# Kernel optimization log

Hardware: AMD Instinct MI355X
Metric: run time of the kernel (lower is better)

Reference implementation:

```python
import jax, jax.numpy as jnp
import numpy as np

E, N, D, H = 600000, 100000, 128, 128
LN_EPS = 1e-5


def setup_inputs() -> dict:
    key = jax.random.key(0)
    ks = jax.random.split(key, 10)
    inp = {
        "efeat": jax.random.normal(ks[0], (E, D), dtype=jnp.float32),
        "nfeat": jax.random.normal(ks[1], (N, D), dtype=jnp.float32),
        "src_idx": jax.random.randint(ks[2], (E,), 0, N, dtype=jnp.int64) if jax.config.jax_enable_x64 else jax.random.randint(ks[2], (E,), 0, N, dtype=jnp.int32),
        "dst_idx": jax.random.randint(ks[3], (E,), 0, N, dtype=jnp.int32),
        # MLP params: Linear(3D -> H) + SiLU, Linear(H -> D), LayerNorm(D)
        "W1": jax.random.normal(ks[4], (3 * D, H), dtype=jnp.float32) / np.sqrt(3 * D),
        "b1": jnp.zeros((H,), dtype=jnp.float32),
        "W2": jax.random.normal(ks[5], (H, D), dtype=jnp.float32) / np.sqrt(H),
        "b2": jnp.zeros((D,), dtype=jnp.float32),
        "ln_scale": jnp.ones((D,), dtype=jnp.float32),
        "ln_bias": jnp.zeros((D,), dtype=jnp.float32),
    }
    return inp


def _layernorm(x, scale, bias):
    mu = jnp.mean(x, axis=-1, keepdims=True)
    var = jnp.mean(jnp.square(x - mu), axis=-1, keepdims=True)
    return (x - mu) * jax.lax.rsqrt(var + LN_EPS) * scale + bias


def reference(efeat, nfeat, src_idx, dst_idx, W1, b1, W2, b2, ln_scale, ln_bias):
    # Gather per-edge source/destination node features (irregular access).
    src = nfeat[src_idx]              # [E, D]
    dst = nfeat[dst_idx]              # [E, D]
    # TMLP: equivalent to concat([efeat, src, dst]) @ W1; expressed as split GEMMs
    # so no [E, 3D] concat buffer is materialized.
    Wf, Ws, Wd = W1[:D], W1[D:2 * D], W1[2 * D:]
    h = efeat @ Wf + src @ Ws + dst @ Wd + b1   # [E, H]
    h = jax.nn.silu(h)
    y = h @ W2 + b2                              # [E, D]
    y = _layernorm(y, ln_scale, ln_bias)
    efeat_new = y + efeat                        # residual add
    return (efeat_new, nfeat)
```

## Files before the change

### kernel.cpp

```cpp
#include <hip/hip_runtime.h>
#include <stdint.h>

#define E_N 600000
#define N_N 100000

typedef short short8   __attribute__((ext_vector_type(8)));
typedef short short8a  __attribute__((ext_vector_type(8), may_alias));
typedef float floatx2  __attribute__((ext_vector_type(2)));
typedef float floatx4  __attribute__((ext_vector_type(4)));
typedef float floatx16 __attribute__((ext_vector_type(16)));
typedef float floatx4a __attribute__((ext_vector_type(4), may_alias));
typedef float floatx8a __attribute__((ext_vector_type(8), may_alias));
typedef unsigned int uintx2  __attribute__((ext_vector_type(2)));
typedef unsigned int uintx4  __attribute__((ext_vector_type(4)));
typedef unsigned int uintx4a __attribute__((ext_vector_type(4), may_alias));
typedef __bf16 bf16x4 __attribute__((ext_vector_type(4)));
typedef __bf16 bf16x8 __attribute__((ext_vector_type(8)));

static __device__ __forceinline__ unsigned short f2bf(float f){
  unsigned u = __builtin_bit_cast(unsigned, f);
  unsigned rnd = 0x7fffu + ((u >> 16) & 1u);
  return (unsigned short)((u + rnd) >> 16);
}
static __device__ __forceinline__ unsigned pk2(float a, float b){
  floatx2 f; f[0] = a; f[1] = b;
  typedef __bf16 bf16x2 __attribute__((ext_vector_type(2)));
  return __builtin_bit_cast(unsigned, __builtin_convertvector(f, bf16x2));
}

__global__ void prep_weights(const float* __restrict__ W1, const float* __restrict__ W2,
                             unsigned short* __restrict__ wall){
  int i = blockIdx.x * 256 + threadIdx.x;
  int c, k, win; float v;
  if (i < 384 * 128){
    c = i / 384; k = i - c * 384; win = k >> 6;
    v = W1[k * 128 + c];
  } else {
    int j = i - 384 * 128;
    c = j >> 7; k = j & 127; win = 6 + (k >> 6);
    v = W2[k * 128 + c];
  }
  int kp = k & 63;
  wall[win * 8192 + (c * 32 + ((kp >> 1) ^ ((c & 7) << 2))) * 2 + (kp & 1)] = f2bf(v);
}

__global__ void prep_nfeat(const float* __restrict__ nf,
                           unsigned* __restrict__ nfbu,
                           float* __restrict__ out2){
  const int total = N_N * 128 / 4;
  int stride = gridDim.x * blockDim.x;
  for (int i = blockIdx.x * blockDim.x + threadIdx.x; i < total; i += stride){
    float4 v = reinterpret_cast<const float4*>(nf)[i];
    reinterpret_cast<float4*>(out2)[i] = v;
    nfbu[2 * i]     = pk2(v.x, v.y);
    nfbu[2 * i + 1] = pk2(v.z, v.w);
  }
}

static __device__ __forceinline__ void glds16(void* lds, const void* g){
  __builtin_amdgcn_global_load_lds((const __attribute__((address_space(1))) unsigned int*)g,
                                   (__attribute__((address_space(3))) unsigned int*)lds,
                                   16, 0, 0);
}

__global__ __launch_bounds__(256, 3) void fused_edge(
    const float* __restrict__ efeat,
    const int* __restrict__ src_idx, const int* __restrict__ dst_idx,
    const unsigned short* __restrict__ nfb,
    const unsigned short* __restrict__ wall,
    const float* __restrict__ b1, const float* __restrict__ b2,
    const float* __restrict__ lns, const float* __restrict__ lnb,
    float* __restrict__ out)
{
  __shared__ __align__(16) unsigned char smem[34816];
  unsigned int* wbuf  = (unsigned int*)smem;
  float*        cmisc = (float*)(smem + 32768);

  const int tid  = threadIdx.x;
  const int w    = tid >> 6;
  const int lane = tid & 63;
  const int rl   = lane & 31;
  const int hi   = lane >> 5;
  const int swz  = (rl & 7) << 2;

  auto stageW = [&](int b, int win){
    const unsigned char* src = (const unsigned char*)wall + win * 16384;
    #pragma unroll
    for (int rnd = 0; rnd < 4; ++rnd){
      int off = rnd * 4096 + tid * 16;
      glds16(smem + b * 16384 + off, src + off);
    }
  };

  stageW(0, 0);
  cmisc[tid]       = tid < 128 ? b1[tid]  : b2[tid - 128];
  cmisc[tid + 256] = tid < 128 ? lns[tid] : lnb[tid - 128];

  const int e0 = blockIdx.x * 128 + w * 32 + rl;
  const int ec = e0 < E_N ? e0 : (E_N - 1);
  int si = src_idx[ec], di = dst_idx[ec];
  si = si < 0 ? 0 : (si >= N_N ? N_N - 1 : si);
  di = di < 0 ? 0 : (di >= N_N ? N_N - 1 : di);

  auto ldE = [&](int ks8) -> short8 {
    floatx8a f = *reinterpret_cast<const floatx8a*>(efeat + (size_t)ec * 128 + ks8 * 16 + hi * 8);
    return __builtin_bit_cast(short8, __builtin_convertvector(f, bf16x8));
  };
  auto ldG = [&](int row, int ks8) -> short8 {
    return *reinterpret_cast<const short8a*>(nfb + (size_t)row * 128 + ks8 * 16 + hi * 8);
  };

  short8 xe[8], xc[4], xn[4];
  #pragma unroll
  for (int ks8 = 0; ks8 < 8; ++ks8) xe[ks8] = ldE(ks8);
  #pragma unroll
  for (int k = 0; k < 4; ++k) xc[k] = ldG(si, k);

  __syncthreads();

  auto loadW = [&](int b, int m, int ks) -> short8 {
    uintx4a v = *reinterpret_cast<const uintx4a*>(
        &wbuf[b * 4096 + (32 * m + rl) * 32 + ((ks * 8 + hi * 4) ^ swz)]);
    return __builtin_bit_cast(short8, v);
  };

  floatx16 acc1[4];
  #pragma unroll
  for (int mt = 0; mt < 4; ++mt)
    #pragma unroll
    for (int q = 0; q < 16; ++q) acc1[mt][q] = 0.f;

  auto g1win = [&](int b, const short8* xs){
    #pragma unroll
    for (int ks = 0; ks < 4; ++ks){
      #pragma unroll
      for (int mt = 0; mt < 4; ++mt){
        short8 wf = loadW(b, mt, ks);
        acc1[mt] = __builtin_amdgcn_mfma_f32_32x32x16_bf16(wf, xs[ks], acc1[mt], 0, 0, 0);
      }
    }
  };

  stageW(1, 1);
  #pragma unroll
  for (int k = 0; k < 4; ++k) xn[k] = ldG(si, 4 + k);
  g1win(0, xe);
  __syncthreads();

  stageW(0, 2);
  g1win(1, xe + 4);
  __syncthreads();

  stageW(1, 3);
  g1win(0, xc);
  #pragma unroll
  for (int k = 0; k < 4; ++k) xc[k] = ldG(di, k);
  __syncthreads();

  stageW(0, 4);
  g1win(1, xn);
  #pragma unroll
  for (int k = 0; k < 4; ++k) xn[k] = ldG(di, 4 + k);
  __syncthreads();

  stageW(1, 5);
  g1win(0, xc);
  __syncthreads();

  stageW(0, 6);
  g1win(1, xn);
  __syncthreads();

  short8 hfr[8];
  #pragma unroll
  for (int mt = 0; mt < 4; ++mt){
    floatx4 sv[4];
    #pragma unroll
    for (int p = 0; p < 4; ++p){
      floatx4 bb = *reinterpret_cast<const floatx4a*>(&cmisc[32 * mt + 8 * p + 4 * hi]);
      #pragma unroll
      for (int i = 0; i < 4; ++i){
        float xx = acc1[mt][4 * p + i] + bb[i];
        sv[p][i] = xx * __builtin_amdgcn_rcpf(1.f + __expf(-xx));
      }
    }
    #pragma unroll
    for (int k1 = 0; k1 < 2; ++k1){
      uintx2 P0 = __builtin_bit_cast(uintx2, __builtin_convertvector(sv[2 * k1],     bf16x4));
      uintx2 P1 = __builtin_bit_cast(uintx2, __builtin_convertvector(sv[2 * k1 + 1], bf16x4));
      unsigned sA = hi ? P0[0] : P1[0];
      unsigned sB = hi ? P0[1] : P1[1];
      unsigned rA = __shfl_xor(sA, 32);
      unsigned rB = __shfl_xor(sB, 32);
      uintx4 u;
      u[0] = hi ? rA : P0[0];
      u[1] = hi ? rB : P0[1];
      u[2] = hi ? P1[0] : rA;
      u[3] = hi ? P1[1] : rB;
      hfr[2 * mt + k1] = __builtin_bit_cast(short8, u);
    }
  }

  uintx2 rk[8], rr[8];
  #pragma unroll
  for (int ks = 0; ks < 8; ++ks){
    uintx4 u = __builtin_bit_cast(uintx4, xe[ks]);
    unsigned sA = hi ? u[0] : u[2];
    unsigned sB = hi ? u[1] : u[3];
    rr[ks][0] = __shfl_xor(sA, 32);
    rr[ks][1] = __shfl_xor(sB, 32);
    rk[ks][0] = hi ? u[2] : u[0];
    rk[ks][1] = hi ? u[3] : u[1];
  }

  floatx16 acc2[4];
  #pragma unroll
  for (int mo = 0; mo < 4; ++mo)
    #pragma unroll
    for (int q = 0; q < 16; ++q) acc2[mo][q] = 0.f;

  stageW(1, 7);
  #pragma unroll
  for (int ks = 0; ks < 4; ++ks)
    #pragma unroll
    for (int mo = 0; mo < 4; ++mo)
      acc2[mo] = __builtin_amdgcn_mfma_f32_32x32x16_bf16(loadW(0, mo, ks), hfr[ks], acc2[mo], 0, 0, 0);
  __syncthreads();
  #pragma unroll
  for (int ks = 0; ks < 4; ++ks)
    #pragma unroll
    for (int mo = 0; mo < 4; ++mo)
      acc2[mo] = __builtin_amdgcn_mfma_f32_32x32x16_bf16(loadW(1, mo, ks), hfr[4 + ks], acc2[mo], 0, 0, 0);

  float s1 = 0.f, s2 = 0.f;
  #pragma unroll
  for (int mt = 0; mt < 4; ++mt)
    #pragma unroll
    for (int p = 0; p < 4; ++p){
      floatx4 bb = *reinterpret_cast<const floatx4a*>(&cmisc[128 + 32 * mt + 8 * p + 4 * hi]);
      #pragma unroll
      for (int i = 0; i < 4; ++i){
        float v = acc2[mt][4 * p + i] + bb[i];
        s1 += v; s2 += v * v;
      }
    }
  s1 += __shfl_xor(s1, 32); s2 += __shfl_xor(s2, 32);

  float mu   = s1 * (1.f / 128.f);
  float var  = s2 * (1.f / 128.f) - mu * mu;
  var = var > 0.f ? var : 0.f;
  float rstd = __builtin_amdgcn_rsqf(var + 1e-5f);

  if (e0 < E_N){
    float* op = out + (size_t)e0 * 128;
    #pragma unroll
    for (int mt = 0; mt < 4; ++mt)
      #pragma unroll
      for (int p = 0; p < 4; ++p){
        int c = 32 * mt + 8 * p + 4 * hi;
        floatx4 bb = *reinterpret_cast<const floatx4a*>(&cmisc[128 + c]);
        floatx4 ls = *reinterpret_cast<const floatx4a*>(&cmisc[256 + c]);
        floatx4 lb = *reinterpret_cast<const floatx4a*>(&cmisc[384 + c]);
        const int ks = 2 * mt + (p >> 1);
        uintx2 pk_ = ((p & 1) == hi) ? rk[ks] : rr[ks];
        floatx4 o4;
        #pragma unroll
        for (int i = 0; i < 4; ++i){
          unsigned dwv = pk_[i >> 1];
          float ef = __builtin_bit_cast(float, (i & 1) ? (dwv & 0xffff0000u) : (dwv << 16));
          o4[i] = (acc2[mt][4 * p + i] + bb[i] - mu) * rstd * ls[i] + lb[i] + ef;
        }
        *reinterpret_cast<floatx4a*>(op + c) = o4;
      }
  }
}

extern "C" void kernel_launch(void* const* d_in, const int* in_sizes, int n_in,
                              void* d_out, int out_size, void* d_ws, size_t ws_size,
                              hipStream_t stream){
  const float* efeat = (const float*)d_in[0];
  const float* nfeat = (const float*)d_in[1];
  const int*   srci  = (const int*)d_in[2];
  const int*   dsti  = (const int*)d_in[3];
  const float* W1    = (const float*)d_in[4];
  const float* b1    = (const float*)d_in[5];
  const float* W2    = (const float*)d_in[6];
  const float* b2    = (const float*)d_in[7];
  const float* lns   = (const float*)d_in[8];
  const float* lnb   = (const float*)d_in[9];
  float* out = (float*)d_out;

  char* ws = (char*)d_ws;
  unsigned short* wall = (unsigned short*)ws;
  unsigned short* nfb  = (unsigned short*)(ws + 131072);

  prep_weights<<<(384 * 128 + 128 * 128) / 256, 256, 0, stream>>>(W1, W2, wall);
  prep_nfeat<<<2048, 256, 0, stream>>>(nfeat, (unsigned*)nfb, out + (size_t)E_N * 128);

  int blocks = (E_N + 127) / 128;
  fused_edge<<<blocks, 256, 0, stream>>>(efeat, srci, dsti, nfb, wall,
                                         b1, b2, lns, lnb, out);
}
```

Before: 231.1 us.

## Triple-buffer weight windows with manual vmcnt barriers and MFMA priority

Grows LDS from two to three 16KB weight buffers so weight staging runs two windows ahead. Full __syncthreads are replaced by s_waitcnt vmcnt(N) plus s_barrier, so outstanding node-feature gathers are not drained at each barrier. The gathers are restructured into two rotating register sets, and s_setprio raises wave priority around MFMA loops. The larger LDS footprint (50KB per block) may limit occupancy under launch_bounds(256,3), and the hand-counted vmcnt values must match the actual number of loads in flight for correctness.

```diff
diff --git a/kernel.cpp b/kernel.cpp
--- a/kernel.cpp
+++ b/kernel.cpp
@@ -28,6 +28,15 @@
   return __builtin_bit_cast(unsigned, __builtin_convertvector(f, bf16x2));
 }
 
+#define WAITBAR(N) do{ \
+  asm volatile("s_waitcnt vmcnt(" #N ")" ::: "memory"); \
+  __builtin_amdgcn_s_barrier(); \
+  asm volatile("" ::: "memory"); }while(0)
+#define BARONLY() do{ \
+  asm volatile("" ::: "memory"); \
+  __builtin_amdgcn_s_barrier(); \
+  asm volatile("" ::: "memory"); }while(0)
+
 __global__ void prep_weights(const float* __restrict__ W1, const float* __restrict__ W2,
                              unsigned short* __restrict__ wall){
   int i = blockIdx.x * 256 + threadIdx.x;
@@ -72,9 +81,9 @@
     const float* __restrict__ lns, const float* __restrict__ lnb,
     float* __restrict__ out)
 {
-  __shared__ __align__(16) unsigned char smem[34816];
+  __shared__ __align__(16) unsigned char smem[51200];
   unsigned int* wbuf  = (unsigned int*)smem;
-  float*        cmisc = (float*)(smem + 32768);
+  float*        cmisc = (float*)(smem + 49152);
 
   const int tid  = threadIdx.x;
   const int w    = tid >> 6;
@@ -93,6 +102,7 @@
   };
 
   stageW(0, 0);
+  stageW(1, 1);
   cmisc[tid]       = tid < 128 ? b1[tid]  : b2[tid - 128];
   cmisc[tid + 256] = tid < 128 ? lns[tid] : lnb[tid - 128];
 
@@ -106,17 +116,16 @@
     floatx8a f = *reinterpret_cast<const floatx8a*>(efeat + (size_t)ec * 128 + ks8 * 16 + hi * 8);
     return __builtin_bit_cast(short8, __builtin_convertvector(f, bf16x8));
   };
-  auto ldG = [&](int row, int ks8) -> short8 {
-    return *reinterpret_cast<const short8a*>(nfb + (size_t)row * 128 + ks8 * 16 + hi * 8);
-  };
-
-  short8 xe[8], xc[4], xn[4];
+
+  short8 xe[8], ga[4], gb[4];
   #pragma unroll
   for (int ks8 = 0; ks8 < 8; ++ks8) xe[ks8] = ldE(ks8);
-  #pragma unroll
-  for (int k = 0; k < 4; ++k) xc[k] = ldG(si, k);
-
-  __syncthreads();
+
+  auto gather4 = [&](short8* dst, int row, int k0){
+    #pragma unroll
+    for (int k = 0; k < 4; ++k)
+      dst[k] = *reinterpret_cast<const short8a*>(nfb + (size_t)row * 128 + (k0 + k) * 16 + hi * 8);
+  };
 
   auto loadW = [&](int b, int m, int ks) -> short8 {
     uintx4a v = *reinterpret_cast<const uintx4a*>(
@@ -131,6 +140,7 @@
     for (int q = 0; q < 16; ++q) acc1[mt][q] = 0.f;
 
   auto g1win = [&](int b, const short8* xs){
+    __builtin_amdgcn_s_setprio(1);
     #pragma unroll
     for (int ks = 0; ks < 4; ++ks){
       #pragma unroll
@@ -139,37 +149,37 @@
         acc1[mt] = __builtin_amdgcn_mfma_f32_32x32x16_bf16(wf, xs[ks], acc1[mt], 0, 0, 0);
       }
     }
-  };
-
-  stageW(1, 1);
-  #pragma unroll
-  for (int k = 0; k < 4; ++k) xn[k] = ldG(si, 4 + k);
+    __builtin_amdgcn_s_setprio(0);
+  };
+
+  WAITBAR(0);
+
+  stageW(2, 2);
   g1win(0, xe);
-  __syncthreads();
-
-  stageW(0, 2);
+  gather4(ga, si, 0);
+
+  BARONLY();
+  stageW(0, 3);
   g1win(1, xe + 4);
-  __syncthreads();
-
-  stageW(1, 3);
-  g1win(0, xc);
-  #pragma unroll
-  for (int k = 0; k < 4; ++k) xc[k] = ldG(di, k);
-  __syncthreads();
-
-  stageW(0, 4);
-  g1win(1, xn);
-  #pragma unroll
-  for (int k = 0; k < 4; ++k) xn[k] = ldG(di, 4 + k);
-  __syncthreads();
-
-  stageW(1, 5);
-  g1win(0, xc);
-  __syncthreads();
-
+  gather4(gb, si, 4);
+
+  WAITBAR(8);
+  stageW(1, 4);
+  g1win(2, ga);
+  gather4(ga, di, 0);
+
+  WAITBAR(8);
+  stageW(2, 5);
+  g1win(0, gb);
+  gather4(gb, di, 4);
+
+  WAITBAR(8);
   stageW(0, 6);
-  g1win(1, xn);
-  __syncthreads();
+  g1win(1, ga);
+
+  WAITBAR(4);
+  stageW(1, 7);
+  g1win(2, gb);
 
   short8 hfr[8];
   #pragma unroll
@@ -219,18 +229,23 @@
     #pragma unroll
     for (int q = 0; q < 16; ++q) acc2[mo][q] = 0.f;
 
-  stageW(1, 7);
+  WAITBAR(4);
+  __builtin_amdgcn_s_setprio(1);
   #pragma unroll
   for (int ks = 0; ks < 4; ++ks)
     #pragma unroll
     for (int mo = 0; mo < 4; ++mo)
       acc2[mo] = __builtin_amdgcn_mfma_f32_32x32x16_bf16(loadW(0, mo, ks), hfr[ks], acc2[mo], 0, 0, 0);
-  __syncthreads();
+  __builtin_amdgcn_s_setprio(0);
+
+  WAITBAR(0);
+  __builtin_amdgcn_s_setprio(1);
   #pragma unroll
   for (int ks = 0; ks < 4; ++ks)
     #pragma unroll
     for (int mo = 0; mo < 4; ++mo)
       acc2[mo] = __builtin_amdgcn_mfma_f32_32x32x16_bf16(loadW(1, mo, ks), hfr[4 + ks], acc2[mo], 0, 0, 0);
+  __builtin_amdgcn_s_setprio(0);
 
   float s1 = 0.f, s2 = 0.f;
   #pragma unroll
```

New measurement: 218.2 us, median of 2. -5.6%, faster.
